# Kernel optimization log

Hardware: AMD Instinct MI355X
Metric: run time of the kernel (lower is better)

## Reference

```python
import jax, jax.numpy as jnp
import numpy as np

N = 100000; E = 1600000; G = 512; L = 1000
FXD = 4; FXT = 5; H = 64; NOUT = 2

def setup_inputs() -> dict:
    key = jax.random.key(0)
    ks = jax.random.split(key, 16)
    x = jax.random.normal(ks[0], (N, FXD), dtype=jnp.float32)
    edge_index = jax.random.randint(ks[1], (2, E), 0, N, dtype=jnp.int64)
    # contiguous, non-empty graph assignment (sorted)
    batch = jnp.minimum(jnp.arange(N, dtype=jnp.int64) // (N // G), G - 1)
    target = jax.random.normal(ks[2], (G, L, FXT), dtype=jnp.float32)
    def lin(k, fi, fo):
        s = 1.0 / np.sqrt(fi)
        k1, k2 = jax.random.split(k)
        return (jax.random.uniform(k1, (fi, fo), jnp.float32, -s, s),
                jax.random.uniform(k2, (fo,), jnp.float32, -s, s))
    W1, b1 = lin(ks[3], FXD, H)
    W2, b2 = lin(ks[4], H, 2 * H)
    Wg, bg = lin(ks[5], 2 * H, H)
    s = 1.0 / np.sqrt(FXT * 3)
    Wc = jax.random.uniform(ks[6], (H, FXT, 3), jnp.float32, -s, s)  # OIH
    bc = jax.random.uniform(ks[7], (H,), jnp.float32, -s, s)
    Wt, bt = lin(ks[8], H, H)
    Wf, bf = lin(ks[9], 2 * H, H)
    Wo, bo = lin(ks[10], H, NOUT)
    return dict(x=x, edge_index=edge_index, batch=batch, target=target,
                W1=W1, b1=b1, W2=W2, b2=b2, Wg=Wg, bg=bg,
                Wc=Wc, bc=bc, Wt=Wt, bt=bt, Wf=Wf, bf=bf, Wo=Wo, bo=bo)

def _gcn_prep(edge_index):
    # add self-loops, compute symmetric normalization (PyG gcn_norm)
    loops = jnp.arange(N, dtype=edge_index.dtype)
    row = jnp.concatenate([edge_index[0], loops])
    col = jnp.concatenate([edge_index[1], loops])
    deg = jax.ops.segment_sum(jnp.ones_like(col, dtype=jnp.float32), col, num_segments=N)
    dis = jnp.where(deg > 0, jax.lax.rsqrt(deg), 0.0)
    norm = dis[row] * dis[col]  # [E+N]
    return row, col, norm

def _gcn_conv(h, row, col, norm):
    # gather-scale-scatter aggregation
    msg = h[row] * norm[:, None]
    return jax.ops.segment_sum(msg, col, num_segments=N)

def reference(x, edge_index, batch, target, W1, b1, W2, b2, Wg, bg, Wc, bc, Wt, bt, Wf, bf, Wo, bo):
    row, col, norm = _gcn_prep(edge_index)
    h = jax.nn.relu(_gcn_conv(x @ W1, row, col, norm) + b1)
    h = jax.nn.relu(_gcn_conv(h @ W2, row, col, norm) + b2)
    g = jax.ops.segment_max(h, batch, num_segments=G)  # global_max_pool [G, 2H]
    g = g @ Wg + bg  # dropout = identity (eval)
    t = jnp.transpose(target, (0, 2, 1))  # [G, FXT, L]
    t = jax.lax.conv_general_dilated(t, Wc, (1,), 'VALID',
                                     dimension_numbers=('NCH', 'OIH', 'NCH')) + bc[None, :, None]
    t = jax.nn.relu(t)
    t = jnp.max(t, axis=-1)  # AdaptiveMaxPool1d(1) [G, H]
    t = t @ Wt + bt
    xc = jnp.concatenate([g, t], axis=1)
    xc = jax.nn.relu(xc @ Wf + bf)
    return xc @ Wo + bo
```

## Files before the change

kernel.cpp:

```cpp
#include <hip/hip_runtime.h>
#include <hip/hip_bf16.h>

constexpr int N   = 100000;
constexpr int E   = 1600000;
constexpr int G   = 512;
constexpr int L   = 1000;
constexpr int NPG = 195;

constexpr int SLOTS = 48;
constexpr int NR2   = 256;
constexpr int RS2   = 391;
constexpr int PCAP2 = 6912;
constexpr int BCH   = 4096;

typedef __attribute__((ext_vector_type(8))) short bf16x8;
typedef __attribute__((ext_vector_type(4))) float f32x4;

__device__ __forceinline__ float bf2f(__hip_bfloat16 b) { return __bfloat162float(b); }
__device__ __forceinline__ float lo_bf(unsigned v) { return __uint_as_float(v << 16); }
__device__ __forceinline__ float hi_bf(unsigned v) { return __uint_as_float(v & 0xFFFF0000u); }
__device__ __forceinline__ unsigned packbf2(float a, float b) {
    __hip_bfloat16 ha = __float2bfloat16(a), hb = __float2bfloat16(b);
    unsigned short ua = *(unsigned short*)&ha, ub = *(unsigned short*)&hb;
    return (unsigned)ua | ((unsigned)ub << 16);
}


__global__ void k_init(int* __restrict__ pcnt, const float* __restrict__ W2,
                       short* __restrict__ W2hi, short* __restrict__ W2lo) {
    int i = blockIdx.x * 256 + threadIdx.x;
    if (i < NR2) pcnt[i] = 0;
    if (i < 64 * 128) {
        float w = W2[i];
        __hip_bfloat16 h = __float2bfloat16(w);
        float r = w - __bfloat162float(h);
        __hip_bfloat16 l = __float2bfloat16(r);
        W2hi[i] = *(short*)&h;
        W2lo[i] = *(short*)&l;
    }
}


__global__ void __launch_bounds__(256) k_part(
        const int* __restrict__ row, const int* __restrict__ col,
        int* __restrict__ pcnt, unsigned* __restrict__ precs) {
    __shared__ unsigned rec_s[BCH];
    __shared__ unsigned char rr_s[BCH];
    __shared__ int cnt_s[NR2], base_s[NR2], cur_s[NR2];
    int tid = threadIdx.x;
    cnt_s[tid] = 0;
    __syncthreads();
    int e0 = blockIdx.x * BCH;
    int nE = min(BCH, E - e0);
    for (int i = tid; i < nE; i += 256) {
        int c = __builtin_nontemporal_load(col + e0 + i);
        int r = __builtin_nontemporal_load(row + e0 + i);
        int rr = c / RS2;
        rec_s[i] = ((unsigned)r << 9) | (unsigned)(c - rr * RS2);
        rr_s[i] = (unsigned char)rr;
        atomicAdd(&cnt_s[rr], 1);
    }
    __syncthreads();
    base_s[tid] = atomicAdd(&pcnt[tid], cnt_s[tid]);
    cur_s[tid] = 0;
    __syncthreads();
    for (int i = tid; i < nE; i += 256) {
        int rr = rr_s[i];
        int p = base_s[rr] + atomicAdd(&cur_s[rr], 1);
        if (p < PCAP2) precs[rr * PCAP2 + p] = rec_s[i];
    }
}


__global__ void __launch_bounds__(256) k_sort(
        const int* __restrict__ pcnt, const unsigned* __restrict__ precs,
        int* __restrict__ slots, int* __restrict__ cursor, float* __restrict__ dis) {
    __shared__ unsigned recs[PCAP2];
    __shared__ int hist[512], off[512], off2[512], ps[256];
    int tid = threadIdx.x;
    int rr = blockIdx.x;
    int cnt = min(pcnt[rr], PCAP2);
    hist[tid] = 0; hist[tid + 256] = 0;
    __syncthreads();
    const unsigned* pr = precs + rr * PCAP2;
    for (int i = tid; i < cnt; i += 256) {
        unsigned r = pr[i];
        recs[i] = r;
        atomicAdd(&hist[r & 511], 1);
    }
    __syncthreads();
    int h0 = hist[2 * tid], h1 = hist[2 * tid + 1];
    int s = h0 + h1;
    ps[tid] = s;
    __syncthreads();
    for (int d = 1; d < 256; d <<= 1) {
        int v = (tid >= d) ? ps[tid - d] : 0;
        __syncthreads();
        ps[tid] += v;
        __syncthreads();
    }
    int excl = ps[tid] - s;
    off[2 * tid] = excl;       off[2 * tid + 1] = excl + h0;
    off2[2 * tid] = excl;      off2[2 * tid + 1] = excl + h0;
    __syncthreads();
    for (int ln = tid; ln < RS2; ln += 256) {
        int n = rr * RS2 + ln;
        if (n < N) {
            int c = hist[ln];
            dis[n] = rsqrtf((float)c + 1.0f);
            cursor[n] = n * SLOTS + min(c, SLOTS);
        }
    }
    for (int i = tid; i < cnt; i += 256) {
        unsigned r = recs[i];
        int ln = (int)(r & 511u);
        int p = atomicAdd(&off2[ln], 1);
        int j = p - off[ln];
        if (j < SLOTS) slots[(rr * RS2 + ln) * SLOTS + j] = (int)(r >> 9);
    }
}


__global__ void __launch_bounds__(256) k_gxl1(
        const int* __restrict__ cursor, const int* __restrict__ slots,
        const float* __restrict__ dis, const float4* __restrict__ x,
        const float* __restrict__ W1, const float* __restrict__ b1,
        unsigned* __restrict__ h32) {
    __shared__ float ax[256][4];
    __shared__ float w1s[256];
    __shared__ float b1s[64];
    int tid = threadIdx.x;
    w1s[tid] = W1[tid];
    if (tid < 64) b1s[tid] = b1[tid];
    int nb = blockIdx.x * 256;
    int n = nb + tid;
    float4 a = make_float4(0.f, 0.f, 0.f, 0.f);
    if (n < N) {
        int s = n * SLOTS;
        int cnt = cursor[n] - s;
        float dn = dis[n];
        int j = 0;
        for (; j + 4 <= cnt; j += 4) {
            int s0 = slots[s + j], s1 = slots[s + j + 1],
                s2 = slots[s + j + 2], s3 = slots[s + j + 3];
            float w0 = dis[s0], w1 = dis[s1], w2 = dis[s2], w3 = dis[s3];
            float4 v0 = x[s0], v1 = x[s1], v2 = x[s2], v3 = x[s3];
            a.x = fmaf(v0.x, w0, a.x); a.y = fmaf(v0.y, w0, a.y);
            a.z = fmaf(v0.z, w0, a.z); a.w = fmaf(v0.w, w0, a.w);
            a.x = fmaf(v1.x, w1, a.x); a.y = fmaf(v1.y, w1, a.y);
            a.z = fmaf(v1.z, w1, a.z); a.w = fmaf(v1.w, w1, a.w);
            a.x = fmaf(v2.x, w2, a.x); a.y = fmaf(v2.y, w2, a.y);
            a.z = fmaf(v2.z, w2, a.z); a.w = fmaf(v2.w, w2, a.w);
            a.x = fmaf(v3.x, w3, a.x); a.y = fmaf(v3.y, w3, a.y);
            a.z = fmaf(v3.z, w3, a.z); a.w = fmaf(v3.w, w3, a.w);
        }
        for (; j < cnt; j++) {
            int sx = slots[s + j];
            float w = dis[sx];
            float4 v = x[sx];
            a.x = fmaf(v.x, w, a.x); a.y = fmaf(v.y, w, a.y);
            a.z = fmaf(v.z, w, a.z); a.w = fmaf(v.w, w, a.w);
        }
        float4 xs = x[n];
        float sl = dn * dn;
        a.x = fmaf(xs.x, sl, a.x * dn);
        a.y = fmaf(xs.y, sl, a.y * dn);
        a.z = fmaf(xs.z, sl, a.z * dn);
        a.w = fmaf(xs.w, sl, a.w * dn);
    }
    ax[tid][0] = a.x; ax[tid][1] = a.y; ax[tid][2] = a.z; ax[tid][3] = a.w;
    __syncthreads();
    int p = tid & 31, r0 = tid >> 5;
    int f0 = 2 * p, f1 = 2 * p + 1;
    float wA0 = w1s[f0],       wB0 = w1s[f1];
    float wA1 = w1s[64 + f0],  wB1 = w1s[64 + f1];
    float wA2 = w1s[128 + f0], wB2 = w1s[128 + f1];
    float wA3 = w1s[192 + f0], wB3 = w1s[192 + f1];
    float bb0 = b1s[f0], bb1 = b1s[f1];
    #pragma unroll 4
    for (int i = 0; i < 32; i++) {
        int ln = r0 + 8 * i;
        int node = nb + ln;
        if (node >= N) break;
        float v0 = bb0, v1 = bb1;
        float g0 = ax[ln][0], g1 = ax[ln][1], g2 = ax[ln][2], g3 = ax[ln][3];
        v0 = fmaf(g0, wA0, v0); v1 = fmaf(g0, wB0, v1);
        v0 = fmaf(g1, wA1, v0); v1 = fmaf(g1, wB1, v1);
        v0 = fmaf(g2, wA2, v0); v1 = fmaf(g2, wB2, v1);
        v0 = fmaf(g3, wA3, v0); v1 = fmaf(g3, wB3, v1);
        h32[(size_t)node * 32 + p] = packbf2(fmaxf(v0, 0.0f), fmaxf(v1, 0.0f));
    }
}


__global__ void __launch_bounds__(256) k_gather_h(
        const int* __restrict__ cursor, const int* __restrict__ slots,
        const float* __restrict__ dis, const unsigned* __restrict__ h32,
        unsigned* __restrict__ aggh32) {
    __shared__ int   ls[8][SLOTS];
    __shared__ float lw[8][SLOTS];
    __shared__ int   lcnt[8];
    int tid = threadIdx.x;
    int nb = blockIdx.x * 8;
    if (tid < 8) {
        int node = nb + tid;
        lcnt[tid] = (node < N) ? (cursor[node] - node * SLOTS) : 0;
    }
    __syncthreads();
    for (int i = tid; i < 8 * SLOTS; i += 256) {
        int lo = i / SLOTS, j = i % SLOTS;
        if (j < lcnt[lo]) {
            int src = slots[(nb + lo) * SLOTS + j];
            ls[lo][j] = src;
            lw[lo][j] = dis[src];
        }
    }
    __syncthreads();
    int wid = tid >> 6, lane = tid & 63;
    int half = lane >> 5, li = lane & 31;
    int local = wid * 2 + half;
    int n = nb + local;
    if (n >= N) return;
    int cnt = lcnt[local];
    float dn = dis[n];
    float acc0 = 0.0f, acc1 = 0.0f;
    int j = 0;
    for (; j + 8 <= cnt; j += 8) {
        unsigned v[8]; float w[8];
        #pragma unroll
        for (int k = 0; k < 8; k++) {
            int src = ls[local][j + k];
            v[k] = h32[(size_t)src * 32 + li];
            w[k] = lw[local][j + k];
        }
        #pragma unroll
        for (int k = 0; k < 8; k++) {
            acc0 = fmaf(w[k], lo_bf(v[k]), acc0);
            acc1 = fmaf(w[k], hi_bf(v[k]), acc1);
        }
    }
    for (; j < cnt; j++) {
        int src = ls[local][j];
        unsigned v = h32[(size_t)src * 32 + li];
        float w = lw[local][j];
        acc0 = fmaf(w, lo_bf(v), acc0);
        acc1 = fmaf(w, hi_bf(v), acc1);
    }
    unsigned sv = h32[(size_t)n * 32 + li];
    acc0 = fmaf(dn, lo_bf(sv), acc0) * dn;
    acc1 = fmaf(dn, hi_bf(sv), acc1) * dn;
    aggh32[(size_t)n * 32 + li] = packbf2(acc0, acc1);
}


__global__ void __launch_bounds__(256) k_conv(
        const float* __restrict__ target, const float* __restrict__ Wc,
        const float* __restrict__ bc, float* __restrict__ tb) {
    __shared__ float tg[L * 5];
    __shared__ float pm[4 * 64];
    int tid = threadIdx.x;
    int gi = blockIdx.x;
    const float* tsrc = target + (size_t)gi * (L * 5);
    for (int i = tid; i < L * 5; i += 256) tg[i] = tsrc[i];
    __syncthreads();
    int co = tid & 63, rr = tid >> 6;
    float wc[15];
    #pragma unroll
    for (int j = 0; j < 15; j++) wc[j] = Wc[co * 15 + j];
    int p0 = rr * 250;
    int pend = min(p0 + 250, 998);
    float a0 = tg[p0 * 5 + 0], a1 = tg[p0 * 5 + 1], a2 = tg[p0 * 5 + 2],
          a3 = tg[p0 * 5 + 3], a4 = tg[p0 * 5 + 4];
    float b0 = tg[p0 * 5 + 5], b1 = tg[p0 * 5 + 6], b2 = tg[p0 * 5 + 7],
          b3 = tg[p0 * 5 + 8], b4 = tg[p0 * 5 + 9];
    float m = -1e30f;
    for (int p = p0; p < pend; p++) {
        const float* cp = &tg[(p + 2) * 5];
        float c0 = cp[0], c1 = cp[1], c2 = cp[2], c3 = cp[3], c4 = cp[4];
        float v = 0.0f;
        v = fmaf(a0, wc[0],  v); v = fmaf(b0, wc[1],  v); v = fmaf(c0, wc[2],  v);
        v = fmaf(a1, wc[3],  v); v = fmaf(b1, wc[4],  v); v = fmaf(c1, wc[5],  v);
        v = fmaf(a2, wc[6],  v); v = fmaf(b2, wc[7],  v); v = fmaf(c2, wc[8],  v);
        v = fmaf(a3, wc[9],  v); v = fmaf(b3, wc[10], v); v = fmaf(c3, wc[11], v);
        v = fmaf(a4, wc[12], v); v = fmaf(b4, wc[13], v); v = fmaf(c4, wc[14], v);
        m = fmaxf(m, v);
        a0 = b0; a1 = b1; a2 = b2; a3 = b3; a4 = b4;
        b0 = c0; b1 = c1; b2 = c2; b3 = c3; b4 = c4;
    }
    pm[rr * 64 + co] = m;
    __syncthreads();
    if (tid < 64) {
        float mm = fmaxf(fmaxf(pm[tid], pm[64 + tid]), fmaxf(pm[128 + tid], pm[192 + tid]));
        tb[gi * 64 + tid] = fmaxf(mm + bc[tid], 0.0f);
    }
}


__global__ void __launch_bounds__(256) k_mfma_pool(
        const __hip_bfloat16* __restrict__ aggh,
        const short* __restrict__ W2hi, const short* __restrict__ W2lo,
        const float* __restrict__ b2, const float* __restrict__ tb,
        const float* __restrict__ Wg, const float* __restrict__ bg,
        const float* __restrict__ Wt, const float* __restrict__ bt,
        const float* __restrict__ Wf, const float* __restrict__ bf,
        const float* __restrict__ Wo, const float* __restrict__ bo,
        float* __restrict__ out) {
    __shared__ float gvec[128], ts[64], g2s[64], t2s[64], xcs[64];
    int tid = threadIdx.x;
    int wid = tid >> 6, lane = tid & 63;
    int m = lane & 15, quad = lane >> 4;
    int gi = blockIdx.x;
    int n0 = gi * NPG;
    int n1 = (gi == G - 1) ? N : n0 + NPG;
    int cb0 = wid * 32, cb1 = cb0 + 16;
    bf16x8 bh[2][2], bl[2][2];
    #pragma unroll
    for (int t = 0; t < 2; t++) {
        int cb = cb0 + t * 16;
        #pragma unroll
        for (int ks = 0; ks < 2; ks++) {
            bf16x8 hh, ll;
            #pragma unroll
            for (int j = 0; j < 8; j++) {
                int k = ks * 32 + quad * 8 + j;
                hh[j] = W2hi[k * 128 + cb + m];
                ll[j] = W2lo[k * 128 + cb + m];
            }
            bh[t][ks] = hh; bl[t][ks] = ll;
        }
    }
    float bias0 = b2[cb0 + m], bias1 = b2[cb1 + m];
    const short* ah = (const short*)aggh;
    float mx0 = 0.0f, mx1 = 0.0f;
    bf16x8 a0, a1;
    {
        const short* p = ah + (size_t)(n0 + m) * 64 + quad * 8;
        a0 = *(const bf16x8*)p;
        a1 = *(const bf16x8*)(p + 32);
    }
    for (int bn = n0; bn < n1; bn += 16) {
        bf16x8 na0 = a0, na1 = a1;
        if (bn + 16 < n1) {
            const short* p = ah + (size_t)(bn + 16 + m) * 64 + quad * 8;
            na0 = *(const bf16x8*)p;
            na1 = *(const bf16x8*)(p + 32);
        }
        f32x4 acc0 = {0.f, 0.f, 0.f, 0.f};
        f32x4 acc1 = {0.f, 0.f, 0.f, 0.f};
        acc0 = __builtin_amdgcn_mfma_f32_16x16x32_bf16(a0, bh[0][0], acc0, 0, 0, 0);
        acc0 = __builtin_amdgcn_mfma_f32_16x16x32_bf16(a1, bh[0][1], acc0, 0, 0, 0);
        acc0 = __builtin_amdgcn_mfma_f32_16x16x32_bf16(a0, bl[0][0], acc0, 0, 0, 0);
        acc0 = __builtin_amdgcn_mfma_f32_16x16x32_bf16(a1, bl[0][1], acc0, 0, 0, 0);
        acc1 = __builtin_amdgcn_mfma_f32_16x16x32_bf16(a0, bh[1][0], acc1, 0, 0, 0);
        acc1 = __builtin_amdgcn_mfma_f32_16x16x32_bf16(a1, bh[1][1], acc1, 0, 0, 0);
        acc1 = __builtin_amdgcn_mfma_f32_16x16x32_bf16(a0, bl[1][0], acc1, 0, 0, 0);
        acc1 = __builtin_amdgcn_mfma_f32_16x16x32_bf16(a1, bl[1][1], acc1, 0, 0, 0);
        int rb = bn + quad * 4;
        #pragma unroll
        for (int r = 0; r < 4; r++) {
            float v0 = fmaxf(acc0[r] + bias0, 0.0f);
            float v1 = fmaxf(acc1[r] + bias1, 0.0f);
            if (rb + r < n1) {
                mx0 = fmaxf(mx0, v0);
                mx1 = fmaxf(mx1, v1);
            }
        }
        a0 = na0; a1 = na1;
    }
    mx0 = fmaxf(mx0, __shfl_xor(mx0, 16));
    mx0 = fmaxf(mx0, __shfl_xor(mx0, 32));
    mx1 = fmaxf(mx1, __shfl_xor(mx1, 16));
    mx1 = fmaxf(mx1, __shfl_xor(mx1, 32));
    if (quad == 0) {
        gvec[cb0 + m] = mx0;
        gvec[cb1 + m] = mx1;
    }
    __syncthreads();
    if (wid == 0) {
        ts[lane] = tb[gi * 64 + lane];
        float a = bg[lane];
        #pragma unroll 8
        for (int k = 0; k < 128; k++) a = fmaf(gvec[k], Wg[k * 64 + lane], a);
        float b = bt[lane];
        #pragma unroll 8
        for (int k = 0; k < 64; k++) b = fmaf(ts[k], Wt[k * 64 + lane], b);
        g2s[lane] = a;
        t2s[lane] = b;
        float c = bf[lane];
        #pragma unroll 8
        for (int k = 0; k < 64; k++) c = fmaf(g2s[k], Wf[k * 64 + lane], c);
        #pragma unroll 8
        for (int k = 0; k < 64; k++) c = fmaf(t2s[k], Wf[(64 + k) * 64 + lane], c);
        xcs[lane] = fmaxf(c, 0.0f);
        if (lane < 2) {
            float o = bo[lane];
            for (int k = 0; k < 64; k++) o = fmaf(xcs[k], Wo[k * 2 + lane], o);
            out[gi * 2 + lane] = o;
        }
    }
}


extern "C" void kernel_launch(void* const* d_in, const int* in_sizes, int n_in,
                              void* d_out, int out_size, void* d_ws, size_t ws_size,
                              hipStream_t stream) {
    const float* x      = (const float*)d_in[0];
    const int*   ei     = (const int*)d_in[1];
    const float* target = (const float*)d_in[3];
    const float* W1 = (const float*)d_in[4];
    const float* b1 = (const float*)d_in[5];
    const float* W2 = (const float*)d_in[6];
    const float* b2 = (const float*)d_in[7];
    const float* Wg = (const float*)d_in[8];
    const float* bg = (const float*)d_in[9];
    const float* Wc = (const float*)d_in[10];
    const float* bc = (const float*)d_in[11];
    const float* Wt = (const float*)d_in[12];
    const float* bt = (const float*)d_in[13];
    const float* Wf = (const float*)d_in[14];
    const float* bf = (const float*)d_in[15];
    const float* Wo = (const float*)d_in[16];
    const float* bo = (const float*)d_in[17];
    float* out = (float*)d_out;

    const int* row = ei;
    const int* col = ei + E;

    char* base = (char*)d_ws;
    size_t o = 0;
    auto alloc = [&](size_t bytes) -> void* {
        void* p = base + o;
        o = (o + bytes + 255) & ~(size_t)255;
        return p;
    };
    int*      cursor = (int*)     alloc((size_t)N * 4);
    float*    dis    = (float*)   alloc((size_t)N * 4);
    int*      slots  = (int*)     alloc((size_t)N * SLOTS * 4);
    int*      pcnt   = (int*)     alloc(NR2 * 4);
    unsigned* precs  = (unsigned*)alloc((size_t)NR2 * PCAP2 * 4);
    __hip_bfloat16* h    = (__hip_bfloat16*)alloc((size_t)N * 64 * 2);
    __hip_bfloat16* aggh = (__hip_bfloat16*)alloc((size_t)N * 64 * 2);
    short*    W2hi   = (short*)   alloc((size_t)64 * 128 * 2);
    short*    W2lo   = (short*)   alloc((size_t)64 * 128 * 2);
    float*    tb     = (float*)   alloc((size_t)G * 64 * 4);
    (void)    alloc(4096);

    k_init     <<<32, 256, 0, stream>>>(pcnt, W2, W2hi, W2lo);
    k_part     <<<(E + BCH - 1) / BCH, 256, 0, stream>>>(row, col, pcnt, precs);
    k_sort     <<<NR2, 256, 0, stream>>>(pcnt, precs, slots, cursor, dis);
    k_gxl1     <<<(N + 255) / 256, 256, 0, stream>>>(cursor, slots, dis,
                                                     (const float4*)x, W1, b1,
                                                     (unsigned*)h);
    k_gather_h <<<(N + 7) / 8, 256, 0, stream>>>(cursor, slots, dis,
                                                 (const unsigned*)h, (unsigned*)aggh);
    k_conv     <<<G, 256, 0, stream>>>(target, Wc, bc, tb);
    k_mfma_pool<<<G, 256, 0, stream>>>(aggh, W2hi, W2lo, b2, tb, Wg, bg, Wt, bt,
                                       Wf, bf, Wo, bo, out);
}
```

Measured before the change: 261.5 us.

## Fuse edge partition, target conv and W2 split into one heterogeneous launch

Merges the edge-partition kernel, the 1D conv/max-pool over the target sequence and the W2 hi/lo split into a single launch whose blocks branch on blockIdx, with a union of shared memory. The pcnt zeroing moves to a memset. This removes two kernel launches and lets the independent conv work overlap with the atomic-heavy partition pass. Separately, the gather kernel packs source index and weight into one int2 in LDS and raises the unroll to 16 with a 4-wide tail, to get more loads in flight. The union sizes shared memory to the larger layout, which may lower occupancy for the partition blocks.

```diff
diff --git a/kernel.cpp b/kernel.cpp
--- a/kernel.cpp
+++ b/kernel.cpp
@@ -12,6 +12,7 @@
 constexpr int RS2   = 391;
 constexpr int PCAP2 = 6912;
 constexpr int BCH   = 4096;
+constexpr int NBP   = (E + BCH - 1) / BCH;
 
 typedef __attribute__((ext_vector_type(8))) short bf16x8;
 typedef __attribute__((ext_vector_type(4))) float f32x4;
@@ -25,49 +26,93 @@
     return (unsigned)ua | ((unsigned)ub << 16);
 }
 
-
-__global__ void k_init(int* __restrict__ pcnt, const float* __restrict__ W2,
-                       short* __restrict__ W2hi, short* __restrict__ W2lo) {
-    int i = blockIdx.x * 256 + threadIdx.x;
-    if (i < NR2) pcnt[i] = 0;
-    if (i < 64 * 128) {
-        float w = W2[i];
-        __hip_bfloat16 h = __float2bfloat16(w);
-        float r = w - __bfloat162float(h);
-        __hip_bfloat16 l = __float2bfloat16(r);
-        W2hi[i] = *(short*)&h;
-        W2lo[i] = *(short*)&l;
-    }
-}
-
-
-__global__ void __launch_bounds__(256) k_part(
+struct SMPart { unsigned rec[BCH]; unsigned char rr[BCH];
+                int cnt[NR2]; int base[NR2]; int cur[NR2]; };
+struct SMConv { float tg[L * 5]; float pm[4 * 64]; };
+
+
+__global__ void __launch_bounds__(256) k_part_conv(
         const int* __restrict__ row, const int* __restrict__ col,
-        int* __restrict__ pcnt, unsigned* __restrict__ precs) {
-    __shared__ unsigned rec_s[BCH];
-    __shared__ unsigned char rr_s[BCH];
-    __shared__ int cnt_s[NR2], base_s[NR2], cur_s[NR2];
+        int* __restrict__ pcnt, unsigned* __restrict__ precs,
+        const float* __restrict__ target, const float* __restrict__ Wc,
+        const float* __restrict__ bc, float* __restrict__ tb,
+        const float* __restrict__ W2, short* __restrict__ W2hi,
+        short* __restrict__ W2lo) {
+    __shared__ __align__(16) char smbuf[sizeof(SMPart) > sizeof(SMConv)
+                                        ? sizeof(SMPart) : sizeof(SMConv)];
     int tid = threadIdx.x;
-    cnt_s[tid] = 0;
-    __syncthreads();
-    int e0 = blockIdx.x * BCH;
-    int nE = min(BCH, E - e0);
-    for (int i = tid; i < nE; i += 256) {
-        int c = __builtin_nontemporal_load(col + e0 + i);
-        int r = __builtin_nontemporal_load(row + e0 + i);
-        int rr = c / RS2;
-        rec_s[i] = ((unsigned)r << 9) | (unsigned)(c - rr * RS2);
-        rr_s[i] = (unsigned char)rr;
-        atomicAdd(&cnt_s[rr], 1);
-    }
-    __syncthreads();
-    base_s[tid] = atomicAdd(&pcnt[tid], cnt_s[tid]);
-    cur_s[tid] = 0;
-    __syncthreads();
-    for (int i = tid; i < nE; i += 256) {
-        int rr = rr_s[i];
-        int p = base_s[rr] + atomicAdd(&cur_s[rr], 1);
-        if (p < PCAP2) precs[rr * PCAP2 + p] = rec_s[i];
+    int bid = blockIdx.x;
+    if (bid < NBP) {
+        SMPart& sp = *reinterpret_cast<SMPart*>(smbuf);
+        sp.cnt[tid] = 0;
+        __syncthreads();
+        int e0 = bid * BCH;
+        int nE = min(BCH, E - e0);
+        for (int i = tid; i < nE; i += 256) {
+            int c = __builtin_nontemporal_load(col + e0 + i);
+            int r = __builtin_nontemporal_load(row + e0 + i);
+            int rr = c / RS2;
+            sp.rec[i] = ((unsigned)r << 9) | (unsigned)(c - rr * RS2);
+            sp.rr[i] = (unsigned char)rr;
+            atomicAdd(&sp.cnt[rr], 1);
+        }
+        __syncthreads();
+        sp.base[tid] = atomicAdd(&pcnt[tid], sp.cnt[tid]);
+        sp.cur[tid] = 0;
+        __syncthreads();
+        for (int i = tid; i < nE; i += 256) {
+            int rr = sp.rr[i];
+            int p = sp.base[rr] + atomicAdd(&sp.cur[rr], 1);
+            if (p < PCAP2) precs[rr * PCAP2 + p] = sp.rec[i];
+        }
+    } else if (bid < NBP + G) {
+        SMConv& sc = *reinterpret_cast<SMConv*>(smbuf);
+        int gi = bid - NBP;
+        const float* tsrc = target + (size_t)gi * (L * 5);
+        for (int i = tid; i < L * 5; i += 256) sc.tg[i] = tsrc[i];
+        __syncthreads();
+        int co = tid & 63, rr = tid >> 6;
+        float wc[15];
+        #pragma unroll
+        for (int j = 0; j < 15; j++) wc[j] = Wc[co * 15 + j];
+        const float* tg = sc.tg;
+        int p0 = rr * 250;
+        int pend = min(p0 + 250, 998);
+        float a0 = tg[p0 * 5 + 0], a1 = tg[p0 * 5 + 1], a2 = tg[p0 * 5 + 2],
+              a3 = tg[p0 * 5 + 3], a4 = tg[p0 * 5 + 4];
+        float b0 = tg[p0 * 5 + 5], b1 = tg[p0 * 5 + 6], b2 = tg[p0 * 5 + 7],
+              b3 = tg[p0 * 5 + 8], b4 = tg[p0 * 5 + 9];
+        float m = -1e30f;
+        for (int p = p0; p < pend; p++) {
+            const float* cp = &tg[(p + 2) * 5];
+            float c0 = cp[0], c1 = cp[1], c2 = cp[2], c3 = cp[3], c4 = cp[4];
+            float v = 0.0f;
+            v = fmaf(a0, wc[0],  v); v = fmaf(b0, wc[1],  v); v = fmaf(c0, wc[2],  v);
+            v = fmaf(a1, wc[3],  v); v = fmaf(b1, wc[4],  v); v = fmaf(c1, wc[5],  v);
+            v = fmaf(a2, wc[6],  v); v = fmaf(b2, wc[7],  v); v = fmaf(c2, wc[8],  v);
+            v = fmaf(a3, wc[9],  v); v = fmaf(b3, wc[10], v); v = fmaf(c3, wc[11], v);
+            v = fmaf(a4, wc[12], v); v = fmaf(b4, wc[13], v); v = fmaf(c4, wc[14], v);
+            m = fmaxf(m, v);
+            a0 = b0; a1 = b1; a2 = b2; a3 = b3; a4 = b4;
+            b0 = c0; b1 = c1; b2 = c2; b3 = c3; b4 = c4;
+        }
+        sc.pm[rr * 64 + co] = m;
+        __syncthreads();
+        if (tid < 64) {
+            float mm = fmaxf(fmaxf(sc.pm[tid], sc.pm[64 + tid]),
+                             fmaxf(sc.pm[128 + tid], sc.pm[192 + tid]));
+            tb[gi * 64 + tid] = fmaxf(mm + bc[tid], 0.0f);
+        }
+    } else {
+        int i = (bid - NBP - G) * 256 + tid;
+        if (i < 64 * 128) {
+            float w = W2[i];
+            __hip_bfloat16 h = __float2bfloat16(w);
+            float r = w - __bfloat162float(h);
+            __hip_bfloat16 l = __float2bfloat16(r);
+            W2hi[i] = *(short*)&h;
+            W2lo[i] = *(short*)&l;
+        }
     }
 }
 
@@ -197,9 +242,8 @@
         const int* __restrict__ cursor, const int* __restrict__ slots,
         const float* __restrict__ dis, const unsigned* __restrict__ h32,
         unsigned* __restrict__ aggh32) {
-    __shared__ int   ls[8][SLOTS];
-    __shared__ float lw[8][SLOTS];
-    __shared__ int   lcnt[8];
+    __shared__ int2 lsw[8][SLOTS];
+    __shared__ int  lcnt[8];
     int tid = threadIdx.x;
     int nb = blockIdx.x * 8;
     if (tid < 8) {
@@ -208,11 +252,10 @@
     }
     __syncthreads();
     for (int i = tid; i < 8 * SLOTS; i += 256) {
-        int lo = i / SLOTS, j = i % SLOTS;
+        int lo = i / SLOTS, j = i - lo * SLOTS;
         if (j < lcnt[lo]) {
             int src = slots[(nb + lo) * SLOTS + j];
-            ls[lo][j] = src;
-            lw[lo][j] = dis[src];
+            lsw[lo][j] = make_int2(src, __float_as_int(dis[src]));
         }
     }
     __syncthreads();
@@ -225,24 +268,38 @@
     float dn = dis[n];
     float acc0 = 0.0f, acc1 = 0.0f;
     int j = 0;
-    for (; j + 8 <= cnt; j += 8) {
-        unsigned v[8]; float w[8];
-        #pragma unroll
-        for (int k = 0; k < 8; k++) {
-            int src = ls[local][j + k];
-            v[k] = h32[(size_t)src * 32 + li];
-            w[k] = lw[local][j + k];
-        }
-        #pragma unroll
-        for (int k = 0; k < 8; k++) {
+    for (; j + 16 <= cnt; j += 16) {
+        unsigned v[16]; float w[16];
+        #pragma unroll
+        for (int k = 0; k < 16; k++) {
+            int2 e = lsw[local][j + k];
+            v[k] = h32[(size_t)e.x * 32 + li];
+            w[k] = __int_as_float(e.y);
+        }
+        #pragma unroll
+        for (int k = 0; k < 16; k++) {
             acc0 = fmaf(w[k], lo_bf(v[k]), acc0);
             acc1 = fmaf(w[k], hi_bf(v[k]), acc1);
         }
     }
+    for (; j + 4 <= cnt; j += 4) {
+        unsigned v[4]; float w[4];
+        #pragma unroll
+        for (int k = 0; k < 4; k++) {
+            int2 e = lsw[local][j + k];
+            v[k] = h32[(size_t)e.x * 32 + li];
+            w[k] = __int_as_float(e.y);
+        }
+        #pragma unroll
+        for (int k = 0; k < 4; k++) {
+            acc0 = fmaf(w[k], lo_bf(v[k]), acc0);
+            acc1 = fmaf(w[k], hi_bf(v[k]), acc1);
+        }
+    }
     for (; j < cnt; j++) {
-        int src = ls[local][j];
-        unsigned v = h32[(size_t)src * 32 + li];
-        float w = lw[local][j];
+        int2 e = lsw[local][j];
+        unsigned v = h32[(size_t)e.x * 32 + li];
+        float w = __int_as_float(e.y);
         acc0 = fmaf(w, lo_bf(v), acc0);
         acc1 = fmaf(w, hi_bf(v), acc1);
     }
@@ -250,49 +307,6 @@
     acc0 = fmaf(dn, lo_bf(sv), acc0) * dn;
     acc1 = fmaf(dn, hi_bf(sv), acc1) * dn;
     aggh32[(size_t)n * 32 + li] = packbf2(acc0, acc1);
-}
-
-
-__global__ void __launch_bounds__(256) k_conv(
-        const float* __restrict__ target, const float* __restrict__ Wc,
-        const float* __restrict__ bc, float* __restrict__ tb) {
-    __shared__ float tg[L * 5];
-    __shared__ float pm[4 * 64];
-    int tid = threadIdx.x;
-    int gi = blockIdx.x;
-    const float* tsrc = target + (size_t)gi * (L * 5);
-    for (int i = tid; i < L * 5; i += 256) tg[i] = tsrc[i];
-    __syncthreads();
-    int co = tid & 63, rr = tid >> 6;
-    float wc[15];
-    #pragma unroll
-    for (int j = 0; j < 15; j++) wc[j] = Wc[co * 15 + j];
-    int p0 = rr * 250;
-    int pend = min(p0 + 250, 998);
-    float a0 = tg[p0 * 5 + 0], a1 = tg[p0 * 5 + 1], a2 = tg[p0 * 5 + 2],
-          a3 = tg[p0 * 5 + 3], a4 = tg[p0 * 5 + 4];
-    float b0 = tg[p0 * 5 + 5], b1 = tg[p0 * 5 + 6], b2 = tg[p0 * 5 + 7],
-          b3 = tg[p0 * 5 + 8], b4 = tg[p0 * 5 + 9];
-    float m = -1e30f;
-    for (int p = p0; p < pend; p++) {
-        const float* cp = &tg[(p + 2) * 5];
-        float c0 = cp[0], c1 = cp[1], c2 = cp[2], c3 = cp[3], c4 = cp[4];
-        float v = 0.0f;
-        v = fmaf(a0, wc[0],  v); v = fmaf(b0, wc[1],  v); v = fmaf(c0, wc[2],  v);
-        v = fmaf(a1, wc[3],  v); v = fmaf(b1, wc[4],  v); v = fmaf(c1, wc[5],  v);
-        v = fmaf(a2, wc[6],  v); v = fmaf(b2, wc[7],  v); v = fmaf(c2, wc[8],  v);
-        v = fmaf(a3, wc[9],  v); v = fmaf(b3, wc[10], v); v = fmaf(c3, wc[11], v);
-        v = fmaf(a4, wc[12], v); v = fmaf(b4, wc[13], v); v = fmaf(c4, wc[14], v);
-        m = fmaxf(m, v);
-        a0 = b0; a1 = b1; a2 = b2; a3 = b3; a4 = b4;
-        b0 = c0; b1 = c1; b2 = c2; b3 = c3; b4 = c4;
-    }
-    pm[rr * 64 + co] = m;
-    __syncthreads();
-    if (tid < 64) {
-        float mm = fmaxf(fmaxf(pm[tid], pm[64 + tid]), fmaxf(pm[128 + tid], pm[192 + tid]));
-        tb[gi * 64 + tid] = fmaxf(mm + bc[tid], 0.0f);
-    }
 }
 
 
@@ -445,15 +459,16 @@
     float*    tb     = (float*)   alloc((size_t)G * 64 * 4);
     (void)    alloc(4096);
 
-    k_init     <<<32, 256, 0, stream>>>(pcnt, W2, W2hi, W2lo);
-    k_part     <<<(E + BCH - 1) / BCH, 256, 0, stream>>>(row, col, pcnt, precs);
+    (void)hipMemsetAsync(pcnt, 0, NR2 * 4, stream);
+    k_part_conv<<<NBP + G + 32, 256, 0, stream>>>(row, col, pcnt, precs,
+                                                  target, Wc, bc, tb,
+                                                  W2, W2hi, W2lo);
     k_sort     <<<NR2, 256, 0, stream>>>(pcnt, precs, slots, cursor, dis);
     k_gxl1     <<<(N + 255) / 256, 256, 0, stream>>>(cursor, slots, dis,
                                                      (const float4*)x, W1, b1,
                                                      (unsigned*)h);
     k_gather_h <<<(N + 7) / 8, 256, 0, stream>>>(cursor, slots, dis,
                                                  (const unsigned*)h, (unsigned*)aggh);
-    k_conv     <<<G, 256, 0, stream>>>(target, Wc, bc, tb);
     k_mfma_pool<<<G, 256, 0, stream>>>(aggh, W2hi, W2lo, b2, tb, Wg, bg, Wt, bt,
                                        Wf, bf, Wo, bo, out);
 }
```

Measured after the change: 237.6 us. 1.1x faster.
